# Kernel optimization log

Measured on AMD Instinct MI355X. Metric: run time of the kernel, lower is better.

Reference implementation:

```python
import jax, jax.numpy as jnp
import numpy as np

EPS_IN = 1e-5   # torch InstanceNorm2d default eps
EPS_VAR = 1e-6  # clamp floor on attention-weighted variance


def _inorm(x):
    # x: (b, c, t); InstanceNorm2d with affine=False normalizes over spatial dims
    m = x.mean(axis=-1, keepdims=True)
    v = x.var(axis=-1, keepdims=True)  # biased variance, matches torch eval-mode IN
    return (x - m) / jnp.sqrt(v + EPS_IN)


def setup_inputs() -> dict:
    key = jax.random.key(0)
    ks = jax.random.split(key, 9)
    b, t, d = 4, 4096, 256
    sc = 1.0 / np.sqrt(d).astype(np.float32)
    return {
        "fc": jax.random.normal(ks[0], (b, t, d), jnp.float32),
        "fs": jax.random.normal(ks[1], (b, t, d), jnp.float32),
        "fcs": jax.random.normal(ks[2], (b, t, d), jnp.float32),
        "Wf": jax.random.normal(ks[3], (d, d), jnp.float32) * sc,
        "bf": jax.random.normal(ks[4], (d,), jnp.float32) * 0.01,
        "Wg": jax.random.normal(ks[5], (d, d), jnp.float32) * sc,
        "bg": jax.random.normal(ks[6], (d,), jnp.float32) * 0.01,
        "Wh": jax.random.normal(ks[7], (d, d), jnp.float32) * sc,
        "bh": jax.random.normal(ks[8], (d,), jnp.float32) * 0.01,
    }


def reference(fc, fs, fcs, Wf, bf, Wg, bg, Wh, bh):
    # (b, t, d) -> channel-first flat (b, d, t); 1x1 conv == per-token linear
    fc_t = jnp.swapaxes(fc, 1, 2)
    fs_t = jnp.swapaxes(fs, 1, 2)
    fcs_t = jnp.swapaxes(fcs, 1, 2)

    Q = jnp.einsum('oc,bct->bto', Wf, _inorm(fc_t)) + bf                 # (b,t,d)
    K = jnp.einsum('oc,bct->bot', Wg, _inorm(fs_t)) + bg[None, :, None]  # (b,d,t)
    V = jnp.einsum('oc,bct->bto', Wh, fs_t) + bh                         # (b,t,d)

    A = jax.nn.softmax(jnp.einsum('btd,bdu->btu', Q, K), axis=-1)        # (b,t,t)
    M = jnp.einsum('btu,bud->btd', A, V)                                 # mean
    Var = jnp.einsum('btu,bud->btd', A, V * V) - M * M                   # E[v^2]-E[v]^2
    S = jnp.sqrt(jnp.maximum(Var, EPS_VAR))

    out_t = jnp.swapaxes(S, 1, 2) * _inorm(fcs_t) + jnp.swapaxes(M, 1, 2)  # (b,d,t)
    return jnp.swapaxes(out_t, 1, 2)  # (b, t, d)
```

## Files before the change

### kernel.cpp

```cpp
#include <hip/hip_runtime.h>
#include <math.h>

#define B 4
#define T 4096
#define D 256
#define NCH 16
#define CHT (T / NCH)
#define KC 32
#define NCHUNK (T / KC)

typedef __attribute__((ext_vector_type(8))) _Float16 half8;
typedef __attribute__((ext_vector_type(4))) _Float16 half4;
typedef __attribute__((ext_vector_type(4))) float f32x4;

__global__ __launch_bounds__(256) void k_prep(
    const float* __restrict__ fc, const float* __restrict__ fs,
    const float* __restrict__ fcs, float* __restrict__ part,
    const float* __restrict__ Wf, const float* __restrict__ Wg,
    const float* __restrict__ Wh, _Float16* __restrict__ Whi,
    _Float16* __restrict__ Wlo)
{
    int blk = blockIdx.x;
    if (blk < 192) {
        int tensor = blk / (B * NCH);
        int rem = blk % (B * NCH);
        int b = rem / NCH, ch = rem % NCH;
        const float* x = (tensor == 0) ? fc : ((tensor == 1) ? fs : fcs);
        int c = threadIdx.x;
        const float* p = x + ((size_t)b * T + (size_t)ch * CHT) * D + c;
        float s = 0.f, ss = 0.f;
        for (int t = 0; t < CHT; ++t) {
            float v = p[(size_t)t * D];
            s += v; ss += v * v;
        }
        float* o = part + (((size_t)tensor * B + b) * NCH + ch) * 2 * D;
        o[c] = s;
        o[D + c] = ss;
    } else {
        int base = (blk - 192) * 2048;
        #pragma unroll
        for (int i = 0; i < 8; ++i) {
            int idx = base + threadIdx.x + i * 256;
            int which = idx >> 16, rc = idx & 65535;
            const float* Wsrc = (which == 0) ? Wf : ((which == 1) ? Wg : Wh);
            float v = Wsrc[rc];
            _Float16 h = (_Float16)v;
            float l = v - (float)h;
            Whi[idx] = h;
            Wlo[idx] = (_Float16)l;
        }
    }
}

__global__ __launch_bounds__(256) void k_gemm3(
    const float* __restrict__ fc, const float* __restrict__ fs,
    const _Float16* __restrict__ Whi, const _Float16* __restrict__ Wlo,
    const float* __restrict__ bf, const float* __restrict__ bg,
    const float* __restrict__ bh, const float* __restrict__ part,
    _Float16* __restrict__ Qg, _Float16* __restrict__ Kg,
    _Float16* __restrict__ oV, _Float16* __restrict__ oV2h,
    _Float16* __restrict__ oV2l)
{
    __shared__ _Float16 Xl[64 * 256];
    __shared__ float mean_s[256], rstd_s[256];
    const int which = blockIdx.x >> 8;
    const int m0 = (blockIdx.x & 255) * 64;
    const int b = m0 / T;
    const int tid = threadIdx.x;
    const float* x = (which == 0) ? fc : fs;
    const float* bias = (which == 0) ? bf : ((which == 1) ? bg : bh);
    const _Float16* Wh_ = Whi + which * 65536;
    const _Float16* Wl_ = Wlo + which * 65536;
    const int use_norm = (which != 2);

    if (use_norm) {
        int c = tid;
        const float* pp = part + (((size_t)which * B + b) * NCH) * 2 * D;
        float s = 0.f, ss = 0.f;
        for (int ch = 0; ch < NCH; ++ch) {
            s  += pp[(size_t)ch * 2 * D + c];
            ss += pp[(size_t)ch * 2 * D + D + c];
        }
        float mean = s / (float)T;
        float var  = ss / (float)T - mean * mean;
        mean_s[c] = mean;
        rstd_s[c] = rsqrtf(var + 1e-5f);
    }
    __syncthreads();

    #pragma unroll
    for (int j = 0; j < 16; ++j) {
        int idx = tid + j * 256;
        int m = idx >> 6, c4 = idx & 63;
        float4 v = *(const float4*)(x + ((size_t)(m0 + m)) * D + c4 * 4);
        if (use_norm) {
            int c = c4 * 4;
            v.x = (v.x - mean_s[c + 0]) * rstd_s[c + 0];
            v.y = (v.y - mean_s[c + 1]) * rstd_s[c + 1];
            v.z = (v.z - mean_s[c + 2]) * rstd_s[c + 2];
            v.w = (v.w - mean_s[c + 3]) * rstd_s[c + 3];
        }
        half4 h;
        h[0] = (_Float16)v.x; h[1] = (_Float16)v.y;
        h[2] = (_Float16)v.z; h[3] = (_Float16)v.w;
        *(half4*)&Xl[m * 256 + ((c4 * 4) ^ ((m & 7) << 3))] = h;
    }
    __syncthreads();

    const int l = tid & 63, w = tid >> 6;
    const int lo16 = l & 15, hi4 = l >> 4;
    const int row = w * 16 + lo16;

    float bias_v[16];
    #pragma unroll
    for (int nt = 0; nt < 16; ++nt) bias_v[nt] = bias[nt * 16 + lo16];

    f32x4 acc[16];
    #pragma unroll
    for (int nt = 0; nt < 16; ++nt) acc[nt] = (f32x4){0.f, 0.f, 0.f, 0.f};

    #pragma unroll
    for (int kk = 0; kk < 8; ++kk) {
        half8 a = *(const half8*)&Xl[row * 256 + ((kk * 32 + hi4 * 8) ^ ((row & 7) << 3))];
        #pragma unroll
        for (int nt = 0; nt < 16; ++nt) {
            size_t wo = (size_t)(nt * 16 + lo16) * 256 + kk * 32 + hi4 * 8;
            half8 bhf = *(const half8*)(Wh_ + wo);
            acc[nt] = __builtin_amdgcn_mfma_f32_16x16x32_f16(a, bhf, acc[nt], 0, 0, 0);
            half8 blf = *(const half8*)(Wl_ + wo);
            acc[nt] = __builtin_amdgcn_mfma_f32_16x16x32_f16(a, blf, acc[nt], 0, 0, 0);
        }
    }

    if (which != 2) {
        _Float16* out1 = (which == 0) ? Qg : Kg;
        #pragma unroll
        for (int nt = 0; nt < 16; ++nt)
            #pragma unroll
            for (int r = 0; r < 4; ++r) {
                int t = m0 + w * 16 + hi4 * 4 + r;
                out1[(size_t)t * D + nt * 16 + lo16] = (_Float16)(acc[nt][r] + bias_v[nt]);
            }
    } else {
        int t0 = (m0 % T) + w * 16 + hi4 * 4;
        #pragma unroll
        for (int nt = 0; nt < 16; ++nt) {
            int o = nt * 16 + lo16;
            half4 vh, h4, l4;
            #pragma unroll
            for (int r = 0; r < 4; ++r) {
                float v = acc[nt][r] + bias_v[nt];
                _Float16 vhh = (_Float16)v;
                float f2 = (float)vhh * (float)vhh;
                _Float16 hh = (_Float16)f2;
                float fl = f2 - (float)hh;
                vh[r] = vhh; h4[r] = hh; l4[r] = (_Float16)fl;
            }
            size_t base = ((size_t)b * D + o) * T + t0;
            *(half4*)(oV   + base) = vh;
            *(half4*)(oV2h + base) = h4;
            *(half4*)(oV2l + base) = l4;
        }
    }
}

__global__ __launch_bounds__(512, 1) void k_attn(
    const _Float16* __restrict__ Qg, const _Float16* __restrict__ Kg,
    const _Float16* __restrict__ Vtg, const _Float16* __restrict__ V2hg,
    const _Float16* __restrict__ V2lg, const float* __restrict__ fcs,
    const float* __restrict__ part, float* __restrict__ out)
{
    __shared__ __align__(16) _Float16 Kl [2][32 * 256];
    __shared__ __align__(16) _Float16 Vl [2][256 * 32];
    __shared__ __align__(16) _Float16 V2h[2][256 * 32];
    __shared__ __align__(16) _Float16 V2l[2][256 * 32];
    __shared__ __align__(16) _Float16 Pl [2][64 * 32];
    __shared__ float corr_lds[2][64];
    __shared__ float l_lds[64];
    __shared__ int   flags[2][4];
    __shared__ float mfc_s[256], rfc_s[256];

    const int tid = threadIdx.x;
    const int l = tid & 63;
    const int w = tid >> 6;
    const int swz = (blockIdx.x & 7) * 32 + (blockIdx.x >> 3);
    const int b  = swz >> 6;
    const int q0 = (swz & 63) << 6;
    const int lo16 = l & 15, hi4 = l >> 4;

    const _Float16* KgB  = Kg   + (size_t)b * T * D;
    const _Float16* VtB  = Vtg  + (size_t)b * D * T;
    const _Float16* V2hB = V2hg + (size_t)b * D * T;
    const _Float16* V2lB = V2lg + (size_t)b * D * T;

    if (tid < 256) {
        int c = tid;
        const float* pp = part + (((size_t)2 * B + b) * NCH) * 2 * D;
        float s = 0.f, ss = 0.f;
        for (int ch = 0; ch < NCH; ++ch) {
            s  += pp[(size_t)ch * 2 * D + c];
            ss += pp[(size_t)ch * 2 * D + D + c];
        }
        float mean = s / (float)T;
        float var  = ss / (float)T - mean * mean;
        mfc_s[c] = mean;
        rfc_s[c] = rsqrtf(var + 1e-5f);
    }

    half8 qf[8];
    if (w < 4) {
        const _Float16* qp = Qg + ((size_t)(b * T + q0 + 16 * w + lo16)) * D + hi4 * 8;
        #pragma unroll
        for (int kk = 0; kk < 8; ++kk) qf[kk] = *(const half8*)(qp + kk * 32);
    }

    f32x4 accM[4][2], accE[4][2];
    #pragma unroll
    for (int qs = 0; qs < 4; ++qs)
        #pragma unroll
        for (int jj = 0; jj < 2; ++jj) {
            accM[qs][jj] = (f32x4){0.f, 0.f, 0.f, 0.f};
            accE[qs][jj] = (f32x4){0.f, 0.f, 0.f, 0.f};
        }
    float m_run[4] = {-1e9f, -1e9f, -1e9f, -1e9f};
    float lv[4] = {0.f, 0.f, 0.f, 0.f};

    const int t2 = tid & 255;
    half8 vr[4], vhr[4], vlr[4];

    auto do_pv = [&](int pb) {
        #pragma unroll
        for (int qs = 0; qs < 4; ++qs) {
            if (flags[pb][qs]) {
                #pragma unroll
                for (int r = 0; r < 4; ++r) {
                    float c = corr_lds[pb][qs * 16 + hi4 * 4 + r];
                    accM[qs][0][r] *= c; accM[qs][1][r] *= c;
                    accE[qs][0][r] *= c; accE[qs][1][r] *= c;
                }
            }
        }
        half8 pa[4];
        #pragma unroll
        for (int qs = 0; qs < 4; ++qs) {
            int q = qs * 16 + lo16;
            pa[qs] = *(const half8*)&Pl[pb][q * 32 + ((hi4 ^ (q & 3)) << 3)];
        }
        __builtin_amdgcn_s_setprio(1);
        #pragma unroll
        for (int jj = 0; jj < 2; ++jj) {
            int d = (2 * w + jj) * 16 + lo16;
            int p = d * 32 + ((hi4 ^ ((d >> 1) & 3)) << 3);
            half8 bh  = *(const half8*)&Vl[pb][p];
            half8 b2h = *(const half8*)&V2h[pb][p];
            half8 b2l = *(const half8*)&V2l[pb][p];
            #pragma unroll
            for (int qs = 0; qs < 4; ++qs) {
                accM[qs][jj] = __builtin_amdgcn_mfma_f32_16x16x32_f16(pa[qs], bh,  accM[qs][jj], 0, 0, 0);
                accE[qs][jj] = __builtin_amdgcn_mfma_f32_16x16x32_f16(pa[qs], b2h, accE[qs][jj], 0, 0, 0);
                accE[qs][jj] = __builtin_amdgcn_mfma_f32_16x16x32_f16(pa[qs], b2l, accE[qs][jj], 0, 0, 0);
            }
        }
        __builtin_amdgcn_s_setprio(0);
    };

    if (w >= 4) {
        half8 kr0[4];
        #pragma unroll
        for (int i = 0; i < 4; ++i) {
            int g = t2 + i * 256;
            kr0[i] = *(const half8*)(KgB + (size_t)(g >> 5) * D + (g & 31) * 8);
        }
        #pragma unroll
        for (int i = 0; i < 4; ++i) {
            int g = t2 + i * 256; int d = g >> 2, kg = g & 3;
            size_t off = (size_t)d * T + kg * 8;
            vr[i]  = *(const half8*)(VtB  + off);
            vhr[i] = *(const half8*)(V2hB + off);
            vlr[i] = *(const half8*)(V2lB + off);
        }
        #pragma unroll
        for (int i = 0; i < 4; ++i) {
            int g = t2 + i * 256; int rr = g >> 5, cg = g & 31;
            *(half8*)&Kl[0][rr * 256 + ((cg ^ (rr & 7)) << 3)] = kr0[i];
        }
    }
    __syncthreads();

    for (int kc = 0; kc < NCHUNK; ++kc) {
        const int cb = kc & 1, pb = cb ^ 1;

        if (w < 4) {
            f32x4 c0 = (f32x4){0.f, 0.f, 0.f, 0.f}, c1 = (f32x4){0.f, 0.f, 0.f, 0.f};
            __builtin_amdgcn_s_setprio(1);
            #pragma unroll
            for (int kk = 0; kk < 8; ++kk) {
                int cg = kk * 4 + hi4;
                half8 b0 = *(const half8*)&Kl[cb][lo16 * 256 + ((cg ^ (lo16 & 7)) << 3)];
                half8 b1 = *(const half8*)&Kl[cb][(16 + lo16) * 256 + ((cg ^ ((16 + lo16) & 7)) << 3)];
                c0 = __builtin_amdgcn_mfma_f32_16x16x32_f16(qf[kk], b0, c0, 0, 0, 0);
                c1 = __builtin_amdgcn_mfma_f32_16x16x32_f16(qf[kk], b1, c1, 0, 0, 0);
            }
            __builtin_amdgcn_s_setprio(0);

            if (kc > 0) do_pv(pb);

            float cm[4];
            #pragma unroll
            for (int r = 0; r < 4; ++r) cm[r] = fmaxf(c0[r], c1[r]);
            float tmax = fmaxf(fmaxf(cm[0] - m_run[0], cm[1] - m_run[1]),
                               fmaxf(cm[2] - m_run[2], cm[3] - m_run[3]));
            int flagv = 0;
            if (__any(tmax > 10.f)) {
                flagv = 1;
                float corr[4];
                #pragma unroll
                for (int r = 0; r < 4; ++r) {
                    float rm = cm[r];
                    rm = fmaxf(rm, __shfl_xor(rm, 1));
                    rm = fmaxf(rm, __shfl_xor(rm, 2));
                    rm = fmaxf(rm, __shfl_xor(rm, 4));
                    rm = fmaxf(rm, __shfl_xor(rm, 8));
                    float mn = fmaxf(m_run[r], rm);
                    corr[r] = __expf(m_run[r] - mn);
                    m_run[r] = mn;
                    lv[r] *= corr[r];
                }
                if (lo16 == 0) {
                    #pragma unroll
                    for (int r = 0; r < 4; ++r)
                        corr_lds[cb][w * 16 + hi4 * 4 + r] = corr[r];
                }
            }
            if (l == 0) flags[cb][w] = flagv;

            float p0[4], p1[4];
            #pragma unroll
            for (int r = 0; r < 4; ++r) {
                p0[r] = __expf(c0[r] - m_run[r]);
                p1[r] = __expf(c1[r] - m_run[r]);
                lv[r] += p0[r] + p1[r];
            }
            #pragma unroll
            for (int r = 0; r < 4; ++r) {
                int q = 16 * w + hi4 * 4 + r;
                int ka = lo16, kb = 16 + lo16;
                Pl[cb][q * 32 + (((ka >> 3) ^ (q & 3)) << 3) + (ka & 7)] = (_Float16)p0[r];
                Pl[cb][q * 32 + (((kb >> 3) ^ (q & 3)) << 3) + (kb & 7)] = (_Float16)p1[r];
            }
        } else {
            #pragma unroll
            for (int i = 0; i < 4; ++i) {
                int g = t2 + i * 256; int d = g >> 2, kg = g & 3;
                int p = d * 32 + ((kg ^ ((d >> 1) & 3)) << 3);
                *(half8*)&Vl[cb][p]  = vr[i];
                *(half8*)&V2h[cb][p] = vhr[i];
                *(half8*)&V2l[cb][p] = vlr[i];
            }

            half8 kr[4];
            const bool doK = (kc + 1 < NCHUNK);
            if (doK) {
                int kn = (kc + 1) * KC;
                #pragma unroll
                for (int i = 0; i < 4; ++i) {
                    int g = t2 + i * 256;
                    kr[i] = *(const half8*)(KgB + (size_t)(kn + (g >> 5)) * D + (g & 31) * 8);
                }
                #pragma unroll
                for (int i = 0; i < 4; ++i) {
                    int g = t2 + i * 256; int d = g >> 2, kg = g & 3;
                    size_t off = (size_t)d * T + kn + kg * 8;
                    vr[i]  = *(const half8*)(VtB  + off);
                    vhr[i] = *(const half8*)(V2hB + off);
                    vlr[i] = *(const half8*)(V2lB + off);
                }
            }

            if (kc > 0) do_pv(pb);

            if (doK) {
                #pragma unroll
                for (int i = 0; i < 4; ++i) {
                    int g = t2 + i * 256; int rr = g >> 5, cg = g & 31;
                    *(half8*)&Kl[cb ^ 1][rr * 256 + ((cg ^ (rr & 7)) << 3)] = kr[i];
                }
            }
        }
        __syncthreads();
    }

    do_pv((NCHUNK - 1) & 1);

    if (w < 4) {
        #pragma unroll
        for (int r = 0; r < 4; ++r) {
            float lr = lv[r];
            lr += __shfl_xor(lr, 1);
            lr += __shfl_xor(lr, 2);
            lr += __shfl_xor(lr, 4);
            lr += __shfl_xor(lr, 8);
            if (lo16 == 0) l_lds[w * 16 + hi4 * 4 + r] = lr;
        }
    }
    __syncthreads();

    #pragma unroll
    for (int qs = 0; qs < 4; ++qs) {
        #pragma unroll
        for (int r = 0; r < 4; ++r) {
            float linv = 1.f / l_lds[qs * 16 + hi4 * 4 + r];
            int q = q0 + qs * 16 + hi4 * 4 + r;
            size_t rowb = ((size_t)(b * T + q)) * D;
            #pragma unroll
            for (int jj = 0; jj < 2; ++jj) {
                int d = (2 * w + jj) * 16 + lo16;
                float M  = accM[qs][jj][r] * linv;
                float E2 = accE[qs][jj][r] * linv;
                float S  = sqrtf(fmaxf(E2 - M * M, 1e-6f));
                float f  = fcs[rowb + d];
                out[rowb + d] = S * ((f - mfc_s[d]) * rfc_s[d]) + M;
            }
        }
    }
}

extern "C" void kernel_launch(void* const* d_in, const int* in_sizes, int n_in,
                              void* d_out, int out_size, void* d_ws, size_t ws_size,
                              hipStream_t stream)
{
    const float* fc  = (const float*)d_in[0];
    const float* fs  = (const float*)d_in[1];
    const float* fcs = (const float*)d_in[2];
    const float* Wf  = (const float*)d_in[3];
    const float* bf  = (const float*)d_in[4];
    const float* Wg  = (const float*)d_in[5];
    const float* bg  = (const float*)d_in[6];
    const float* Wh  = (const float*)d_in[7];
    const float* bh  = (const float*)d_in[8];
    float* out = (float*)d_out;

    char* ws = (char*)d_ws;
    float* part  = (float*)(ws + (64 << 10));
    _Float16* Whi = (_Float16*)(ws + (512 << 10));
    _Float16* Wlo = Whi + 3 * 65536;
    _Float16* Qg   = (_Float16*)(ws + (2 << 20));
    _Float16* Kg   = Qg  + (size_t)B * T * D;
    _Float16* Vtg  = Kg  + (size_t)B * T * D;
    _Float16* V2hg = Vtg + (size_t)B * T * D;
    _Float16* V2lg = V2hg + (size_t)B * T * D;

    k_prep<<<288, 256, 0, stream>>>(fc, fs, fcs, part, Wf, Wg, Wh, Whi, Wlo);

    k_gemm3<<<3 * 256, 256, 0, stream>>>(fc, fs, Whi, Wlo, bf, bg, bh, part,
                                         Qg, Kg, Vtg, V2hg, V2lg);

    k_attn<<<B * (T / 64), 512, 0, stream>>>(Qg, Kg, Vtg, V2hg, V2lg, fcs, part, out);
}
```

Before: 317.4 us.

## Load V operands directly from global into registers, drop LDS staging

V, V2-high and V2-low tiles were staged through double-buffered LDS by the producer waves. Now each wave loads its own MFMA B-operand fragments straight from global memory at the start of each chunk, which removes the LDS buffers and the shared-memory write and read traffic. The cost is that global load latency now sits on the critical path inside the loop with no prefetch distance. Each lane also issues its own uncoalesced-ish 16-byte loads, relying on L2 to absorb the reuse across blocks.

New measurement: 338.1 us. 6.5% more time.

```diff
diff --git a/kernel.cpp b/kernel.cpp
--- a/kernel.cpp
+++ b/kernel.cpp
@@ -171,9 +171,6 @@
     const float* __restrict__ part, float* __restrict__ out)
 {
     __shared__ __align__(16) _Float16 Kl [2][32 * 256];
-    __shared__ __align__(16) _Float16 Vl [2][256 * 32];
-    __shared__ __align__(16) _Float16 V2h[2][256 * 32];
-    __shared__ __align__(16) _Float16 V2l[2][256 * 32];
     __shared__ __align__(16) _Float16 Pl [2][64 * 32];
     __shared__ float corr_lds[2][64];
     __shared__ float l_lds[64];
@@ -214,6 +211,11 @@
         for (int kk = 0; kk < 8; ++kk) qf[kk] = *(const half8*)(qp + kk * 32);
     }
 
+    int voff[2];
+    #pragma unroll
+    for (int jj = 0; jj < 2; ++jj)
+        voff[jj] = ((2 * w + jj) * 16 + lo16) * T + hi4 * 8;
+
     f32x4 accM[4][2], accE[4][2];
     #pragma unroll
     for (int qs = 0; qs < 4; ++qs)
@@ -226,9 +228,8 @@
     float lv[4] = {0.f, 0.f, 0.f, 0.f};
 
     const int t2 = tid & 255;
-    half8 vr[4], vhr[4], vlr[4];
-
-    auto do_pv = [&](int pb) {
+
+    auto do_pv = [&](int pb, const half8* bhf, const half8* b2h, const half8* b2l) {
         #pragma unroll
         for (int qs = 0; qs < 4; ++qs) {
             if (flags[pb][qs]) {
@@ -249,16 +250,11 @@
         __builtin_amdgcn_s_setprio(1);
         #pragma unroll
         for (int jj = 0; jj < 2; ++jj) {
-            int d = (2 * w + jj) * 16 + lo16;
-            int p = d * 32 + ((hi4 ^ ((d >> 1) & 3)) << 3);
-            half8 bh  = *(const half8*)&Vl[pb][p];
-            half8 b2h = *(const half8*)&V2h[pb][p];
-            half8 b2l = *(const half8*)&V2l[pb][p];
             #pragma unroll
             for (int qs = 0; qs < 4; ++qs) {
-                accM[qs][jj] = __builtin_amdgcn_mfma_f32_16x16x32_f16(pa[qs], bh,  accM[qs][jj], 0, 0, 0);
-                accE[qs][jj] = __builtin_amdgcn_mfma_f32_16x16x32_f16(pa[qs], b2h, accE[qs][jj], 0, 0, 0);
-                accE[qs][jj] = __builtin_amdgcn_mfma_f32_16x16x32_f16(pa[qs], b2l, accE[qs][jj], 0, 0, 0);
+                accM[qs][jj] = __builtin_amdgcn_mfma_f32_16x16x32_f16(pa[qs], bhf[jj], accM[qs][jj], 0, 0, 0);
+                accE[qs][jj] = __builtin_amdgcn_mfma_f32_16x16x32_f16(pa[qs], b2h[jj], accE[qs][jj], 0, 0, 0);
+                accE[qs][jj] = __builtin_amdgcn_mfma_f32_16x16x32_f16(pa[qs], b2l[jj], accE[qs][jj], 0, 0, 0);
             }
         }
         __builtin_amdgcn_s_setprio(0);
@@ -273,14 +269,6 @@
         }
         #pragma unroll
         for (int i = 0; i < 4; ++i) {
-            int g = t2 + i * 256; int d = g >> 2, kg = g & 3;
-            size_t off = (size_t)d * T + kg * 8;
-            vr[i]  = *(const half8*)(VtB  + off);
-            vhr[i] = *(const half8*)(V2hB + off);
-            vlr[i] = *(const half8*)(V2lB + off);
-        }
-        #pragma unroll
-        for (int i = 0; i < 4; ++i) {
             int g = t2 + i * 256; int rr = g >> 5, cg = g & 31;
             *(half8*)&Kl[0][rr * 256 + ((cg ^ (rr & 7)) << 3)] = kr0[i];
         }
@@ -289,6 +277,17 @@
 
     for (int kc = 0; kc < NCHUNK; ++kc) {
         const int cb = kc & 1, pb = cb ^ 1;
+
+        half8 bhf[2], b2h[2], b2l[2];
+        if (kc > 0) {
+            int kp = (kc - 1) * KC;
+            #pragma unroll
+            for (int jj = 0; jj < 2; ++jj) {
+                bhf[jj] = *(const half8*)(VtB  + kp + voff[jj]);
+                b2h[jj] = *(const half8*)(V2hB + kp + voff[jj]);
+                b2l[jj] = *(const half8*)(V2lB + kp + voff[jj]);
+            }
+        }
 
         if (w < 4) {
             f32x4 c0 = (f32x4){0.f, 0.f, 0.f, 0.f}, c1 = (f32x4){0.f, 0.f, 0.f, 0.f};
@@ -303,7 +302,7 @@
             }
             __builtin_amdgcn_s_setprio(0);
 
-            if (kc > 0) do_pv(pb);
+            if (kc > 0) do_pv(pb, bhf, b2h, b2l);
 
             float cm[4];
             #pragma unroll
@@ -349,15 +348,6 @@
                 Pl[cb][q * 32 + (((kb >> 3) ^ (q & 3)) << 3) + (kb & 7)] = (_Float16)p1[r];
             }
         } else {
-            #pragma unroll
-            for (int i = 0; i < 4; ++i) {
-                int g = t2 + i * 256; int d = g >> 2, kg = g & 3;
-                int p = d * 32 + ((kg ^ ((d >> 1) & 3)) << 3);
-                *(half8*)&Vl[cb][p]  = vr[i];
-                *(half8*)&V2h[cb][p] = vhr[i];
-                *(half8*)&V2l[cb][p] = vlr[i];
-            }
-
             half8 kr[4];
             const bool doK = (kc + 1 < NCHUNK);
             if (doK) {
@@ -367,17 +357,9 @@
                     int g = t2 + i * 256;
                     kr[i] = *(const half8*)(KgB + (size_t)(kn + (g >> 5)) * D + (g & 31) * 8);
                 }
-                #pragma unroll
-                for (int i = 0; i < 4; ++i) {
-                    int g = t2 + i * 256; int d = g >> 2, kg = g & 3;
-                    size_t off = (size_t)d * T + kn + kg * 8;
-                    vr[i]  = *(const half8*)(VtB  + off);
-                    vhr[i] = *(const half8*)(V2hB + off);
-                    vlr[i] = *(const half8*)(V2lB + off);
-                }
-            }
-
-            if (kc > 0) do_pv(pb);
+            }
+
+            if (kc > 0) do_pv(pb, bhf, b2h, b2l);
 
             if (doK) {
                 #pragma unroll
@@ -390,7 +372,17 @@
         __syncthreads();
     }
 
-    do_pv((NCHUNK - 1) & 1);
+    {
+        half8 bhf[2], b2h[2], b2l[2];
+        int kp = (NCHUNK - 1) * KC;
+        #pragma unroll
+        for (int jj = 0; jj < 2; ++jj) {
+            bhf[jj] = *(const half8*)(VtB  + kp + voff[jj]);
+            b2h[jj] = *(const half8*)(V2hB + kp + voff[jj]);
+            b2l[jj] = *(const half8*)(V2lB + kp + voff[jj]);
+        }
+        do_pv((NCHUNK - 1) & 1, bhf, b2h, b2l);
+    }
 
     if (w < 4) {
         #pragma unroll
```
